# Optimization experiments

Hardware: AMD Instinct MI355X
Metric: run time of the kernel (lower is better)

## Reference

```python
import jax, jax.numpy as jnp
import numpy as np

D = 256   # embedding dim d; rows are d+1 = 257
N = 2048  # sequence length n; cols are n+1 = 2049
B = 16

def setup_inputs() -> dict:
    key = jax.random.key(0)
    k_h, k_p, k_q = jax.random.split(key, 3)
    H = jax.random.normal(k_h, (B, D + 1, N + 1), dtype=jnp.float32)
    P = jax.random.normal(k_p, (D + 1, D + 1), dtype=jnp.float32) * 0.01
    Q = jax.random.normal(k_q, (D + 1, D + 1), dtype=jnp.float32) * 0.01
    return {"H": H, "P": P, "Q": Q}

def reference(H, P, Q):
    # H: (B, d+1, n+1)
    n = H.shape[2] - 1
    # HtQH = H^T @ Q @ H : (B, n+1, n+1)
    HtQ = jnp.einsum('bds,de->bse', H, Q)          # (B, n+1, d+1)
    HtQH = jnp.einsum('bse,bet->bst', HtQ, H)      # (B, n+1, n+1)
    # mask M = diag(1,...,1,0): M @ HtQH zeroes the last row
    MHtQH = HtQH.at[:, -1, :].set(0.0)
    PH = jnp.einsum('de,bet->bdt', P, H)           # (B, d+1, n+1)
    attn = jnp.einsum('bds,bst->bdt', PH, MHtQH)   # (B, d+1, n+1)
    return H + attn / n
```

## Files before the change

### kernel.cpp

```cpp
#include <hip/hip_runtime.h>
#include <hip/hip_bf16.h>

#define DP     257
#define NP     2049
#define NSEQ   2048
#define NB     16
#define KLD    288
#define HROWS  320
#define TPITCH 320
#define TROWS  2176
#define KPAD   40

typedef __attribute__((ext_vector_type(8))) short bf16x8;
typedef __attribute__((ext_vector_type(4))) short bf16x4;
typedef __attribute__((ext_vector_type(4))) float f32x4;

__global__ __launch_bounds__(256) void conv_h(const float* __restrict__ H,
                                              __hip_bfloat16* __restrict__ Hb,
                                              __hip_bfloat16* __restrict__ Hbt) {
    const int b  = blockIdx.z;
    const int t0 = blockIdx.x * 64;
    const int e0 = blockIdx.y * 64;
    const float* __restrict__ Hs = H + (size_t)b * DP * NP;
    __hip_bfloat16* __restrict__ Hbb  = Hb  + (size_t)b * HROWS * 2048;
    __hip_bfloat16* __restrict__ Hbtb = Hbt + (size_t)b * TROWS * TPITCH;

    __shared__ float tile[64][65];

    const int tl = threadIdx.x & 63;
    const int er = threadIdx.x >> 6;
#pragma unroll
    for (int r = 0; r < 16; ++r) {
        const int el = er + r * 4;
        const int ge = e0 + el;
        const int gt = t0 + tl;
        float v = 0.f;
        if (ge < DP && gt < NP) v = Hs[(size_t)ge * NP + gt];
        tile[el][tl] = v;
        if (ge < HROWS && gt < 2048) Hbb[(size_t)ge * 2048 + gt] = __float2bfloat16(v);
    }
    __syncthreads();
#pragma unroll
    for (int r = 0; r < 16; ++r) {
        const int ttl = er + r * 4;
        const int gt = t0 + ttl;
        const int ge = e0 + tl;
        if (gt < TROWS && ge < TPITCH) {
            const float v = (ge < KLD) ? tile[tl][ttl] : 0.f;
            Hbtb[(size_t)gt * TPITCH + ge] = __float2bfloat16(v);
        }
    }
}

__global__ __launch_bounds__(256) void conv_pq(const float* __restrict__ P,
                                               const float* __restrict__ Q,
                                               __hip_bfloat16* __restrict__ Pb,
                                               __hip_bfloat16* __restrict__ Qt) {
    const int c0 = blockIdx.x * 64;
    const int r0 = blockIdx.y * 64;
    const int tl = threadIdx.x & 63;
    const int rr = threadIdx.x >> 6;
    __shared__ float tile[64][65];

    if (blockIdx.z == 0) {
#pragma unroll
        for (int r = 0; r < 16; ++r) {
            const int m = r0 + rr + r * 4;
            const int k = c0 + tl;
            float v = (m < DP && k < DP) ? P[m * DP + k] : 0.f;
            if (m < KLD && k < KLD) Pb[m * KLD + k] = __float2bfloat16(v);
        }
    } else {
#pragma unroll
        for (int r = 0; r < 16; ++r) {
            const int k = r0 + rr + r * 4;
            const int n = c0 + tl;
            float v = (k < DP && n < DP) ? Q[k * DP + n] : 0.f;
            tile[k - r0][n - c0] = v;
        }
        __syncthreads();
#pragma unroll
        for (int r = 0; r < 16; ++r) {
            const int k = r0 + tl;
            const int n = c0 + rr + r * 4;
            if (n < KLD && k < KLD) Qt[n * KLD + k] = __float2bfloat16(tile[tl][n - c0]);
        }
    }
}

__global__ __launch_bounds__(512, 4) void gram_staged(const __hip_bfloat16* __restrict__ Hb,
                                                      __hip_bfloat16* __restrict__ G) {
    const int b  = blockIdx.y;
    const int tm = blockIdx.x / 5;
    const int tn = blockIdx.x % 5;
    const int m0 = tm * 64, n0 = tn * 64;
    const int tid = threadIdx.x;
    const int wave = tid >> 6, lane = tid & 63;
    const int lrow = lane & 15, kq = (lane >> 4) * 8;
    const int hw = wave >> 2;
    const int q  = wave & 3;
    const int mh = (q & 1) * 32, nh = (q >> 1) * 32;
    const int hs = tid >> 8;
    const int t2 = tid & 255;
    const int sr = t2 >> 2;
    const int sc = (t2 & 3) * 8;

    __shared__ __align__(16) char smem[2 * 2 * 2 * 64 * KPAD * 2];
    short* As = (short*)smem;
    short* Bs = (short*)(smem + 2 * 2 * 64 * KPAD * 2);
    float* red = (float*)smem;

    const short* __restrict__ base = (const short*)(Hb + (size_t)b * HROWS * 2048);

    auto aoff = [&](int buf, int h, int r) { return ((buf * 2 + h) * 64 + r) * KPAD; };

    f32x4 acc[2][2] = {};

    {
        const int kb = hs * 1024;
        *(bf16x8*)&As[aoff(0, hs, sr) + sc] = *(const bf16x8*)(base + (size_t)(m0 + sr) * 2048 + kb + sc);
        *(bf16x8*)&Bs[aoff(0, hs, sr) + sc] = *(const bf16x8*)(base + (size_t)(n0 + sr) * 2048 + kb + sc);
    }
    __syncthreads();

    for (int kt = 0; kt < 32; ++kt) {
        const int cur = kt & 1, nxt = cur ^ 1;
        if (kt + 1 < 32) {
            const int kb = hs * 1024 + (kt + 1) * 32;
            *(bf16x8*)&As[aoff(nxt, hs, sr) + sc] = *(const bf16x8*)(base + (size_t)(m0 + sr) * 2048 + kb + sc);
            *(bf16x8*)&Bs[aoff(nxt, hs, sr) + sc] = *(const bf16x8*)(base + (size_t)(n0 + sr) * 2048 + kb + sc);
        }
        bf16x8 a0 = *(const bf16x8*)&As[aoff(cur, hw, mh + lrow) + kq];
        bf16x8 a1 = *(const bf16x8*)&As[aoff(cur, hw, mh + 16 + lrow) + kq];
        bf16x8 b0 = *(const bf16x8*)&Bs[aoff(cur, hw, nh + lrow) + kq];
        bf16x8 b1 = *(const bf16x8*)&Bs[aoff(cur, hw, nh + 16 + lrow) + kq];
        acc[0][0] = __builtin_amdgcn_mfma_f32_16x16x32_bf16(a0, b0, acc[0][0], 0, 0, 0);
        acc[0][1] = __builtin_amdgcn_mfma_f32_16x16x32_bf16(a0, b1, acc[0][1], 0, 0, 0);
        acc[1][0] = __builtin_amdgcn_mfma_f32_16x16x32_bf16(a1, b0, acc[1][0], 0, 0, 0);
        acc[1][1] = __builtin_amdgcn_mfma_f32_16x16x32_bf16(a1, b1, acc[1][1], 0, 0, 0);
        __syncthreads();
    }

    const int ccol  = lane & 15;
    const int crow0 = (lane >> 4) * 4;
#pragma unroll
    for (int i = 0; i < 2; ++i)
#pragma unroll
        for (int j = 0; j < 2; ++j)
#pragma unroll
            for (int r = 0; r < 4; ++r)
                red[((wave * 32) + i * 16 + crow0 + r) * 32 + j * 16 + ccol] = acc[i][j][r];
    __syncthreads();

    const int q2  = tid >> 7;
    const int t7  = tid & 127;
    const int row = t7 >> 2;
    const int c8  = (t7 & 3) * 8;
    const int gm = m0 + (q2 & 1) * 32 + row;
    const int gn = n0 + (q2 >> 1) * 32 + c8;
    if (gm < KLD && gn < KLD) {
        __hip_bfloat16 o[8];
#pragma unroll
        for (int t = 0; t < 8; ++t) {
            const float v = red[((q2 * 32) + row) * 32 + c8 + t] +
                            red[(((q2 + 4) * 32) + row) * 32 + c8 + t];
            o[t] = __float2bfloat16((gm < DP && (gn + t) < DP) ? v : 0.f);
        }
        __hip_bfloat16* __restrict__ Gb = G + (size_t)b * KLD * KLD;
        *(bf16x8*)&Gb[gm * KLD + gn] = *(const bf16x8*)o;
    }
}

__global__ __launch_bounds__(256) void mm_sk4(const __hip_bfloat16* __restrict__ A,
                                              const __hip_bfloat16* __restrict__ B,
                                              __hip_bfloat16* __restrict__ C,
                                              int strideA, int strideB) {
    const int b  = blockIdx.y;
    const int tm = blockIdx.x / 9;
    const int tn = blockIdx.x % 9;
    const int s    = threadIdx.x >> 6;
    const int lane = threadIdx.x & 63;
    const int lrow = lane & 15;
    const int koff = (lane >> 4) * 8;
    const short* __restrict__ Ab = (const short*)(A + (size_t)b * strideA);
    const short* __restrict__ Bb = (const short*)(B + (size_t)b * strideB);
    const int m0 = tm * 32, n0 = tn * 32;

    __shared__ float red[4][32][32];

    f32x4 acc[2][2] = {};
    for (int kt = s; kt < 9; kt += 4) {
        const int k0 = kt * 32;
        bf16x8 a0 = *(const bf16x8*)(Ab + (m0 + lrow)      * KLD + k0 + koff);
        bf16x8 a1 = *(const bf16x8*)(Ab + (m0 + 16 + lrow) * KLD + k0 + koff);
        bf16x8 c0 = *(const bf16x8*)(Bb + (n0 + lrow)      * KLD + k0 + koff);
        bf16x8 c1 = *(const bf16x8*)(Bb + (n0 + 16 + lrow) * KLD + k0 + koff);
        acc[0][0] = __builtin_amdgcn_mfma_f32_16x16x32_bf16(a0, c0, acc[0][0], 0, 0, 0);
        acc[0][1] = __builtin_amdgcn_mfma_f32_16x16x32_bf16(a0, c1, acc[0][1], 0, 0, 0);
        acc[1][0] = __builtin_amdgcn_mfma_f32_16x16x32_bf16(a1, c0, acc[1][0], 0, 0, 0);
        acc[1][1] = __builtin_amdgcn_mfma_f32_16x16x32_bf16(a1, c1, acc[1][1], 0, 0, 0);
    }

    const int ccol  = lane & 15;
    const int crow0 = (lane >> 4) * 4;
#pragma unroll
    for (int i = 0; i < 2; ++i)
#pragma unroll
        for (int j = 0; j < 2; ++j)
#pragma unroll
            for (int r = 0; r < 4; ++r)
                red[s][i * 16 + crow0 + r][j * 16 + ccol] = acc[i][j][r];
    __syncthreads();

    const int row = threadIdx.x >> 3;
    const int c4  = (threadIdx.x & 7) * 4;
    float4 v0 = *(const float4*)&red[0][row][c4];
    float4 v1 = *(const float4*)&red[1][row][c4];
    float4 v2 = *(const float4*)&red[2][row][c4];
    float4 v3 = *(const float4*)&red[3][row][c4];
    float sum[4] = {v0.x + v1.x + v2.x + v3.x,
                    v0.y + v1.y + v2.y + v3.y,
                    v0.z + v1.z + v2.z + v3.z,
                    v0.w + v1.w + v2.w + v3.w};
    const int gm = m0 + row;
    const int gn = n0 + c4;
    __hip_bfloat16 o[4];
#pragma unroll
    for (int t = 0; t < 4; ++t) {
        const float v = (gm < DP && (gn + t) < DP) ? sum[t] : 0.f;
        o[t] = __float2bfloat16(v);
    }
    __hip_bfloat16* __restrict__ Cb = C + (size_t)b * KLD * KLD;
    *(bf16x4*)&Cb[gm * KLD + gn] = *(const bf16x4*)o;
}

__global__ __launch_bounds__(256, 4) void attn_v2(const __hip_bfloat16* __restrict__ Kb,
                                                  const __hip_bfloat16* __restrict__ Hbt,
                                                  const float* __restrict__ H,
                                                  float* __restrict__ Out) {
    const int b  = blockIdx.z;
    const int d0 = blockIdx.y * 64;
    const int t0 = blockIdx.x * 128;
    const int tid = threadIdx.x;
    const int wave = tid >> 6, lane = tid & 63;
    const int lrow = lane & 15, kq = (lane >> 4) * 8;
    const int dh = (wave & 1) * 32;
    const int th = (wave >> 1) * 64;
    const int sr = tid >> 2;
    const int sc = (tid & 3) * 8;

    __shared__ __align__(16) char smem[(64 + 128) * KPAD * 2];
    short* As = (short*)smem;
    short* Bs = (short*)(smem + 64 * KPAD * 2);
    float* Ped = (float*)smem;

    const short* __restrict__ Ka = (const short*)(Kb  + (size_t)b * KLD * KLD);
    const short* __restrict__ Ta = (const short*)(Hbt + (size_t)b * TROWS * TPITCH);

    int rA = d0 + sr; if (rA > KLD - 1) rA = KLD - 1;

    f32x4 acc[2][4] = {};

    bf16x8 pA  = *(const bf16x8*)(Ka + (size_t)rA * KLD + sc);
    bf16x8 pB0 = *(const bf16x8*)(Ta + (size_t)(t0 + sr) * TPITCH + sc);
    bf16x8 pB1 = *(const bf16x8*)(Ta + (size_t)(t0 + 64 + sr) * TPITCH + sc);
    *(bf16x8*)&As[sr * KPAD + sc]        = pA;
    *(bf16x8*)&Bs[sr * KPAD + sc]        = pB0;
    *(bf16x8*)&Bs[(64 + sr) * KPAD + sc] = pB1;
    __syncthreads();

    for (int kt = 0; kt < 9; ++kt) {
        if (kt < 8) {
            const int e0 = (kt + 1) * 32;
            pA  = *(const bf16x8*)(Ka + (size_t)rA * KLD + e0 + sc);
            pB0 = *(const bf16x8*)(Ta + (size_t)(t0 + sr) * TPITCH + e0 + sc);
            pB1 = *(const bf16x8*)(Ta + (size_t)(t0 + 64 + sr) * TPITCH + e0 + sc);
        }
        bf16x8 af0 = *(const bf16x8*)&As[(dh + lrow) * KPAD + kq];
        bf16x8 af1 = *(const bf16x8*)&As[(dh + 16 + lrow) * KPAD + kq];
        bf16x8 bfr[4];
#pragma unroll
        for (int j = 0; j < 4; ++j)
            bfr[j] = *(const bf16x8*)&Bs[(th + j * 16 + lrow) * KPAD + kq];
#pragma unroll
        for (int j = 0; j < 4; ++j) {
            acc[0][j] = __builtin_amdgcn_mfma_f32_16x16x32_bf16(af0, bfr[j], acc[0][j], 0, 0, 0);
            acc[1][j] = __builtin_amdgcn_mfma_f32_16x16x32_bf16(af1, bfr[j], acc[1][j], 0, 0, 0);
        }
        __syncthreads();
        if (kt < 8) {
            *(bf16x8*)&As[sr * KPAD + sc]        = pA;
            *(bf16x8*)&Bs[sr * KPAD + sc]        = pB0;
            *(bf16x8*)&Bs[(64 + sr) * KPAD + sc] = pB1;
            __syncthreads();
        }
    }

    const float* __restrict__ Hs = H + (size_t)b * DP * NP;
    float* __restrict__ Ob = Out + (size_t)b * DP * NP;
    const float inv_n = 1.0f / (float)NSEQ;
    const int ccol  = lane & 15;
    const int crow0 = (lane >> 4) * 4;

#pragma unroll
    for (int c = 0; c < 4; ++c) {
        if ((wave & 1) == (c >> 1)) {
            const int i = c & 1;
#pragma unroll
            for (int j = 0; j < 4; ++j)
#pragma unroll
                for (int r = 0; r < 4; ++r)
                    Ped[(crow0 + r) * 132 + th + j * 16 + ccol] = acc[i][j][r];
        }
        __syncthreads();
#pragma unroll
        for (int p = 0; p < 2; ++p) {
            const int row = (tid >> 5) + p * 8;
            const int col = (tid & 31) * 4;
            const int gd = d0 + c * 16 + row;
            if (gd < DP) {
                const float* src = &Ped[row * 132 + col];
                const size_t base = (size_t)gd * NP;
#pragma unroll
                for (int cc = 0; cc < 4; ++cc) {
                    const int gt = t0 + col + cc;
                    if (gt < NP) {
                        const size_t idx = base + gt;
                        Ob[idx] = Hs[idx] + inv_n * src[cc];
                    }
                }
            }
        }
        __syncthreads();
    }
}

extern "C" void kernel_launch(void* const* d_in, const int* in_sizes, int n_in,
                              void* d_out, int out_size, void* d_ws, size_t ws_size,
                              hipStream_t stream) {
    const float* H = (const float*)d_in[0];
    const float* P = (const float*)d_in[1];
    const float* Q = (const float*)d_in[2];
    float* out = (float*)d_out;

    __hip_bfloat16* Hb  = (__hip_bfloat16*)d_ws;
    __hip_bfloat16* Hbt = Hb  + (size_t)NB * HROWS * 2048;
    __hip_bfloat16* G   = Hbt + (size_t)NB * TROWS * TPITCH;
    __hip_bfloat16* Pb  = G   + (size_t)NB * KLD * KLD;
    __hip_bfloat16* Qt  = Pb  + (size_t)KLD * KLD;
    __hip_bfloat16* W   = Hb;
    __hip_bfloat16* Kb  = Hb + (size_t)NB * KLD * KLD;

    conv_pq<<<dim3(5, 5, 2),   256, 0, stream>>>(P, Q, Pb, Qt);
    conv_h <<<dim3(34, 5, NB), 256, 0, stream>>>(H, Hb, Hbt);
    gram_staged<<<dim3(25, NB), 512, 0, stream>>>(Hb, G);
    mm_sk4<<<dim3(81, NB), 256, 0, stream>>>(Pb, G, W, 0, KLD * KLD);
    mm_sk4<<<dim3(81, NB), 256, 0, stream>>>(W, Qt, Kb, KLD * KLD, 0);
    attn_v2<<<dim3(17, 5, NB), 256, 0, stream>>>(Kb, Hbt, H, out);
}
```

Before: 193.4 us.

## Load MFMA fragments directly from global memory and coalesce epilogue stores

The attention kernel no longer stages the K and H^T tiles through shared memory with two barriers per k-step. Each wave now loads its bf16 MFMA fragments straight from global memory into registers, prefetching the next k-slice. The epilogue is reorganised so consecutive threads write consecutive columns, with an unguarded fast path for full column tiles. This removes LDS traffic and synchronisation, but fragments shared across waves are now fetched redundantly from global or L2, and per-lane loads are less coalesced.

After: 203.7 us. 1.05x slower.

```diff
diff --git a/kernel.cpp b/kernel.cpp
--- a/kernel.cpp
+++ b/kernel.cpp
@@ -234,7 +234,7 @@
     *(bf16x4*)&Cb[gm * KLD + gn] = *(const bf16x4*)o;
 }
 
-__global__ __launch_bounds__(256, 4) void attn_v2(const __hip_bfloat16* __restrict__ Kb,
+__global__ __launch_bounds__(256, 4) void attn_v3(const __hip_bfloat16* __restrict__ Kb,
                                                   const __hip_bfloat16* __restrict__ Hbt,
                                                   const float* __restrict__ H,
                                                   float* __restrict__ Out) {
@@ -246,53 +246,52 @@
     const int lrow = lane & 15, kq = (lane >> 4) * 8;
     const int dh = (wave & 1) * 32;
     const int th = (wave >> 1) * 64;
-    const int sr = tid >> 2;
-    const int sc = (tid & 3) * 8;
-
-    __shared__ __align__(16) char smem[(64 + 128) * KPAD * 2];
-    short* As = (short*)smem;
-    short* Bs = (short*)(smem + 64 * KPAD * 2);
-    float* Ped = (float*)smem;
+
+    __shared__ __align__(16) float Ped[16 * 132];
 
     const short* __restrict__ Ka = (const short*)(Kb  + (size_t)b * KLD * KLD);
     const short* __restrict__ Ta = (const short*)(Hbt + (size_t)b * TROWS * TPITCH);
 
-    int rA = d0 + sr; if (rA > KLD - 1) rA = KLD - 1;
+    int ra0 = d0 + dh + lrow;        if (ra0 > KLD - 1) ra0 = KLD - 1;
+    int ra1 = d0 + dh + 16 + lrow;   if (ra1 > KLD - 1) ra1 = KLD - 1;
+    const short* __restrict__ pa0 = Ka + (size_t)ra0 * KLD + kq;
+    const short* __restrict__ pa1 = Ka + (size_t)ra1 * KLD + kq;
+    const short* __restrict__ pb0 = Ta + (size_t)(t0 + th +  0 + lrow) * TPITCH + kq;
+    const short* __restrict__ pb1 = Ta + (size_t)(t0 + th + 16 + lrow) * TPITCH + kq;
+    const short* __restrict__ pb2 = Ta + (size_t)(t0 + th + 32 + lrow) * TPITCH + kq;
+    const short* __restrict__ pb3 = Ta + (size_t)(t0 + th + 48 + lrow) * TPITCH + kq;
 
     f32x4 acc[2][4] = {};
 
-    bf16x8 pA  = *(const bf16x8*)(Ka + (size_t)rA * KLD + sc);
-    bf16x8 pB0 = *(const bf16x8*)(Ta + (size_t)(t0 + sr) * TPITCH + sc);
-    bf16x8 pB1 = *(const bf16x8*)(Ta + (size_t)(t0 + 64 + sr) * TPITCH + sc);
-    *(bf16x8*)&As[sr * KPAD + sc]        = pA;
-    *(bf16x8*)&Bs[sr * KPAD + sc]        = pB0;
-    *(bf16x8*)&Bs[(64 + sr) * KPAD + sc] = pB1;
-    __syncthreads();
+    bf16x8 a0 = *(const bf16x8*)pa0;
+    bf16x8 a1 = *(const bf16x8*)pa1;
+    bf16x8 b0 = *(const bf16x8*)pb0;
+    bf16x8 b1 = *(const bf16x8*)pb1;
+    bf16x8 b2 = *(const bf16x8*)pb2;
+    bf16x8 b3 = *(const bf16x8*)pb3;
 
     for (int kt = 0; kt < 9; ++kt) {
+        bf16x8 na0, na1, nb0, nb1, nb2, nb3;
         if (kt < 8) {
-            const int e0 = (kt + 1) * 32;
-            pA  = *(const bf16x8*)(Ka + (size_t)rA * KLD + e0 + sc);
-            pB0 = *(const bf16x8*)(Ta + (size_t)(t0 + sr) * TPITCH + e0 + sc);
-            pB1 = *(const bf16x8*)(Ta + (size_t)(t0 + 64 + sr) * TPITCH + e0 + sc);
-        }
-        bf16x8 af0 = *(const bf16x8*)&As[(dh + lrow) * KPAD + kq];
-        bf16x8 af1 = *(const bf16x8*)&As[(dh + 16 + lrow) * KPAD + kq];
-        bf16x8 bfr[4];
-#pragma unroll
-        for (int j = 0; j < 4; ++j)
-            bfr[j] = *(const bf16x8*)&Bs[(th + j * 16 + lrow) * KPAD + kq];
-#pragma unroll
-        for (int j = 0; j < 4; ++j) {
-            acc[0][j] = __builtin_amdgcn_mfma_f32_16x16x32_bf16(af0, bfr[j], acc[0][j], 0, 0, 0);
-            acc[1][j] = __builtin_amdgcn_mfma_f32_16x16x32_bf16(af1, bfr[j], acc[1][j], 0, 0, 0);
-        }
-        __syncthreads();
+            const int off = (kt + 1) * 32;
+            na0 = *(const bf16x8*)(pa0 + off);
+            na1 = *(const bf16x8*)(pa1 + off);
+            nb0 = *(const bf16x8*)(pb0 + off);
+            nb1 = *(const bf16x8*)(pb1 + off);
+            nb2 = *(const bf16x8*)(pb2 + off);
+            nb3 = *(const bf16x8*)(pb3 + off);
+        }
+        acc[0][0] = __builtin_amdgcn_mfma_f32_16x16x32_bf16(a0, b0, acc[0][0], 0, 0, 0);
+        acc[0][1] = __builtin_amdgcn_mfma_f32_16x16x32_bf16(a0, b1, acc[0][1], 0, 0, 0);
+        acc[0][2] = __builtin_amdgcn_mfma_f32_16x16x32_bf16(a0, b2, acc[0][2], 0, 0, 0);
+        acc[0][3] = __builtin_amdgcn_mfma_f32_16x16x32_bf16(a0, b3, acc[0][3], 0, 0, 0);
+        acc[1][0] = __builtin_amdgcn_mfma_f32_16x16x32_bf16(a1, b0, acc[1][0], 0, 0, 0);
+        acc[1][1] = __builtin_amdgcn_mfma_f32_16x16x32_bf16(a1, b1, acc[1][1], 0, 0, 0);
+        acc[1][2] = __builtin_amdgcn_mfma_f32_16x16x32_bf16(a1, b2, acc[1][2], 0, 0, 0);
+        acc[1][3] = __builtin_amdgcn_mfma_f32_16x16x32_bf16(a1, b3, acc[1][3], 0, 0, 0);
         if (kt < 8) {
-            *(bf16x8*)&As[sr * KPAD + sc]        = pA;
-            *(bf16x8*)&Bs[sr * KPAD + sc]        = pB0;
-            *(bf16x8*)&Bs[(64 + sr) * KPAD + sc] = pB1;
-            __syncthreads();
+            a0 = na0; a1 = na1;
+            b0 = nb0; b1 = nb1; b2 = nb2; b3 = nb3;
         }
     }
 
@@ -301,6 +300,7 @@
     const float inv_n = 1.0f / (float)NSEQ;
     const int ccol  = lane & 15;
     const int crow0 = (lane >> 4) * 4;
+    const bool fullT = (t0 + 128 <= NP);
 
 #pragma unroll
     for (int c = 0; c < 4; ++c) {
@@ -313,21 +313,30 @@
                     Ped[(crow0 + r) * 132 + th + j * 16 + ccol] = acc[i][j][r];
         }
         __syncthreads();
-#pragma unroll
-        for (int p = 0; p < 2; ++p) {
-            const int row = (tid >> 5) + p * 8;
-            const int col = (tid & 31) * 4;
-            const int gd = d0 + c * 16 + row;
-            if (gd < DP) {
-                const float* src = &Ped[row * 132 + col];
-                const size_t base = (size_t)gd * NP;
-#pragma unroll
-                for (int cc = 0; cc < 4; ++cc) {
-                    const int gt = t0 + col + cc;
-                    if (gt < NP) {
-                        const size_t idx = base + gt;
-                        Ob[idx] = Hs[idx] + inv_n * src[cc];
-                    }
+        const int dchunk = d0 + c * 16;
+        if (fullT) {
+#pragma unroll
+            for (int p = 0; p < 8; ++p) {
+                const int lin = p * 256 + tid;
+                const int row = lin >> 7;
+                const int col = lin & 127;
+                const int gd = dchunk + row;
+                if (gd < DP) {
+                    const size_t idx = (size_t)gd * NP + t0 + col;
+                    Ob[idx] = Hs[idx] + inv_n * Ped[row * 132 + col];
+                }
+            }
+        } else {
+#pragma unroll
+            for (int p = 0; p < 8; ++p) {
+                const int lin = p * 256 + tid;
+                const int row = lin >> 7;
+                const int col = lin & 127;
+                const int gd = dchunk + row;
+                const int gt = t0 + col;
+                if (gd < DP && gt < NP) {
+                    const size_t idx = (size_t)gd * NP + gt;
+                    Ob[idx] = Hs[idx] + inv_n * Ped[row * 132 + col];
                 }
             }
         }
@@ -356,5 +365,5 @@
     gram_staged<<<dim3(25, NB), 512, 0, stream>>>(Hb, G);
     mm_sk4<<<dim3(81, NB), 256, 0, stream>>>(Pb, G, W, 0, KLD * KLD);
     mm_sk4<<<dim3(81, NB), 256, 0, stream>>>(W, Qt, Kb, KLD * KLD, 0);
-    attn_v2<<<dim3(17, 5, NB), 256, 0, stream>>>(Kb, Hbt, H, out);
-}
+    attn_v3<<<dim3(17, 5, NB), 256, 0, stream>>>(Kb, Hbt, H, out);
+}
```

## Shrink attention tile, double-buffer LDS and remap blocks across XCDs

Applied to the files above, without the earlier changes.

The final attention kernel moves from 64x128 to 64x64 output tiles, so there are roughly twice as many blocks and occupancy is raised via launch bounds. The LDS staging becomes double-buffered with one barrier per k-step instead of two. A flat 1D grid is remapped so consecutive block ids are spread across the eight XCD groups. The epilogue writes coalesced 64-wide rows with a fast path for full tiles. The aim is better latency hiding and L2 locality, at the cost of less per-block reuse of the Kb tiles and more blocks.

New measurement: 218.8 us. 1.13x slower.

```diff
diff --git a/kernel.cpp b/kernel.cpp
--- a/kernel.cpp
+++ b/kernel.cpp
@@ -10,6 +10,7 @@
 #define TPITCH 320
 #define TROWS  2176
 #define KPAD   40
+#define KP2    36
 
 typedef __attribute__((ext_vector_type(8))) short bf16x8;
 typedef __attribute__((ext_vector_type(4))) short bf16x4;
@@ -234,66 +235,71 @@
     *(bf16x4*)&Cb[gm * KLD + gn] = *(const bf16x4*)o;
 }
 
-__global__ __launch_bounds__(256, 4) void attn_v2(const __hip_bfloat16* __restrict__ Kb,
+__global__ __launch_bounds__(256, 7) void attn_v4(const __hip_bfloat16* __restrict__ Kb,
                                                   const __hip_bfloat16* __restrict__ Hbt,
                                                   const float* __restrict__ H,
                                                   float* __restrict__ Out) {
-    const int b  = blockIdx.z;
-    const int d0 = blockIdx.y * 64;
-    const int t0 = blockIdx.x * 128;
+    const int id      = blockIdx.x;
+    const int logical = (id & 7) * 330 + (id >> 3);
+    const int y  = logical % 5;
+    const int xb = logical / 5;
+    const int x  = xb % 33;
+    const int b  = xb / 33;
+
+    const int d0 = y * 64;
+    const int t0 = x * 64;
     const int tid = threadIdx.x;
     const int wave = tid >> 6, lane = tid & 63;
     const int lrow = lane & 15, kq = (lane >> 4) * 8;
     const int dh = (wave & 1) * 32;
-    const int th = (wave >> 1) * 64;
+    const int th = (wave >> 1) * 32;
     const int sr = tid >> 2;
     const int sc = (tid & 3) * 8;
 
-    __shared__ __align__(16) char smem[(64 + 128) * KPAD * 2];
-    short* As = (short*)smem;
-    short* Bs = (short*)(smem + 64 * KPAD * 2);
+    __shared__ __align__(16) char smem[2 * 128 * KP2 * 2];
+    short* buf = (short*)smem;
     float* Ped = (float*)smem;
 
     const short* __restrict__ Ka = (const short*)(Kb  + (size_t)b * KLD * KLD);
     const short* __restrict__ Ta = (const short*)(Hbt + (size_t)b * TROWS * TPITCH);
 
     int rA = d0 + sr; if (rA > KLD - 1) rA = KLD - 1;
-
-    f32x4 acc[2][4] = {};
-
-    bf16x8 pA  = *(const bf16x8*)(Ka + (size_t)rA * KLD + sc);
-    bf16x8 pB0 = *(const bf16x8*)(Ta + (size_t)(t0 + sr) * TPITCH + sc);
-    bf16x8 pB1 = *(const bf16x8*)(Ta + (size_t)(t0 + 64 + sr) * TPITCH + sc);
-    *(bf16x8*)&As[sr * KPAD + sc]        = pA;
-    *(bf16x8*)&Bs[sr * KPAD + sc]        = pB0;
-    *(bf16x8*)&Bs[(64 + sr) * KPAD + sc] = pB1;
-    __syncthreads();
+    const short* __restrict__ pA = Ka + (size_t)rA * KLD + sc;
+    const short* __restrict__ pB = Ta + (size_t)(t0 + sr) * TPITCH + sc;
+
+    auto boff = [](int bi, int r) { return (bi * 128 + r) * KP2; };
+
+    {
+        bf16x8 ra = *(const bf16x8*)pA;
+        bf16x8 rb = *(const bf16x8*)pB;
+        *(bf16x8*)&buf[boff(0, sr) + sc]      = ra;
+        *(bf16x8*)&buf[boff(0, 64 + sr) + sc] = rb;
+    }
+    __syncthreads();
+
+    f32x4 acc[2][2] = {};
 
     for (int kt = 0; kt < 9; ++kt) {
+        const int cur = kt & 1;
+        bf16x8 na, nb;
         if (kt < 8) {
-            const int e0 = (kt + 1) * 32;
-            pA  = *(const bf16x8*)(Ka + (size_t)rA * KLD + e0 + sc);
-            pB0 = *(const bf16x8*)(Ta + (size_t)(t0 + sr) * TPITCH + e0 + sc);
-            pB1 = *(const bf16x8*)(Ta + (size_t)(t0 + 64 + sr) * TPITCH + e0 + sc);
-        }
-        bf16x8 af0 = *(const bf16x8*)&As[(dh + lrow) * KPAD + kq];
-        bf16x8 af1 = *(const bf16x8*)&As[(dh + 16 + lrow) * KPAD + kq];
-        bf16x8 bfr[4];
-#pragma unroll
-        for (int j = 0; j < 4; ++j)
-            bfr[j] = *(const bf16x8*)&Bs[(th + j * 16 + lrow) * KPAD + kq];
-#pragma unroll
-        for (int j = 0; j < 4; ++j) {
-            acc[0][j] = __builtin_amdgcn_mfma_f32_16x16x32_bf16(af0, bfr[j], acc[0][j], 0, 0, 0);
-            acc[1][j] = __builtin_amdgcn_mfma_f32_16x16x32_bf16(af1, bfr[j], acc[1][j], 0, 0, 0);
-        }
-        __syncthreads();
+            const int e = (kt + 1) * 32;
+            na = *(const bf16x8*)(pA + e);
+            nb = *(const bf16x8*)(pB + e);
+        }
+        bf16x8 a0 = *(const bf16x8*)&buf[boff(cur, dh + lrow) + kq];
+        bf16x8 a1 = *(const bf16x8*)&buf[boff(cur, dh + 16 + lrow) + kq];
+        bf16x8 b0 = *(const bf16x8*)&buf[boff(cur, 64 + th + lrow) + kq];
+        bf16x8 b1 = *(const bf16x8*)&buf[boff(cur, 64 + th + 16 + lrow) + kq];
+        acc[0][0] = __builtin_amdgcn_mfma_f32_16x16x32_bf16(a0, b0, acc[0][0], 0, 0, 0);
+        acc[0][1] = __builtin_amdgcn_mfma_f32_16x16x32_bf16(a0, b1, acc[0][1], 0, 0, 0);
+        acc[1][0] = __builtin_amdgcn_mfma_f32_16x16x32_bf16(a1, b0, acc[1][0], 0, 0, 0);
+        acc[1][1] = __builtin_amdgcn_mfma_f32_16x16x32_bf16(a1, b1, acc[1][1], 0, 0, 0);
         if (kt < 8) {
-            *(bf16x8*)&As[sr * KPAD + sc]        = pA;
-            *(bf16x8*)&Bs[sr * KPAD + sc]        = pB0;
-            *(bf16x8*)&Bs[(64 + sr) * KPAD + sc] = pB1;
-            __syncthreads();
-        }
+            *(bf16x8*)&buf[boff(cur ^ 1, sr) + sc]      = na;
+            *(bf16x8*)&buf[boff(cur ^ 1, 64 + sr) + sc] = nb;
+        }
+        __syncthreads();
     }
 
     const float* __restrict__ Hs = H + (size_t)b * DP * NP;
@@ -301,33 +307,30 @@
     const float inv_n = 1.0f / (float)NSEQ;
     const int ccol  = lane & 15;
     const int crow0 = (lane >> 4) * 4;
+    const bool fullT = (t0 + 64 <= NP);
 
 #pragma unroll
     for (int c = 0; c < 4; ++c) {
         if ((wave & 1) == (c >> 1)) {
             const int i = c & 1;
 #pragma unroll
-            for (int j = 0; j < 4; ++j)
+            for (int j = 0; j < 2; ++j)
 #pragma unroll
                 for (int r = 0; r < 4; ++r)
-                    Ped[(crow0 + r) * 132 + th + j * 16 + ccol] = acc[i][j][r];
-        }
-        __syncthreads();
-#pragma unroll
-        for (int p = 0; p < 2; ++p) {
-            const int row = (tid >> 5) + p * 8;
-            const int col = (tid & 31) * 4;
-            const int gd = d0 + c * 16 + row;
+                    Ped[(crow0 + r) * 68 + th + j * 16 + ccol] = acc[i][j][r];
+        }
+        __syncthreads();
+        const int dchunk = d0 + c * 16;
+#pragma unroll
+        for (int p = 0; p < 4; ++p) {
+            const int row = p * 4 + (tid >> 6);
+            const int col = tid & 63;
+            const int gd = dchunk + row;
             if (gd < DP) {
-                const float* src = &Ped[row * 132 + col];
-                const size_t base = (size_t)gd * NP;
-#pragma unroll
-                for (int cc = 0; cc < 4; ++cc) {
-                    const int gt = t0 + col + cc;
-                    if (gt < NP) {
-                        const size_t idx = base + gt;
-                        Ob[idx] = Hs[idx] + inv_n * src[cc];
-                    }
+                const int gt = t0 + col;
+                if (fullT || gt < NP) {
+                    const size_t idx = (size_t)gd * NP + gt;
+                    Ob[idx] = Hs[idx] + inv_n * Ped[row * 68 + col];
                 }
             }
         }
@@ -356,5 +359,5 @@
     gram_staged<<<dim3(25, NB), 512, 0, stream>>>(Hb, G);
     mm_sk4<<<dim3(81, NB), 256, 0, stream>>>(Pb, G, W, 0, KLD * KLD);
     mm_sk4<<<dim3(81, NB), 256, 0, stream>>>(W, Qt, Kb, KLD * KLD, 0);
-    attn_v2<<<dim3(17, 5, NB), 256, 0, stream>>>(Kb, Hbt, H, out);
-}
+    attn_v4<<<dim3(33 * 5 * NB), 256, 0, stream>>>(Kb, Hbt, H, out);
+}
```
